# Kernel tuning notes

Measured on AMD Instinct MI355X. Metric: run time of the kernel, lower is better.

The kernel has to match this reference:

```python
import jax, jax.numpy as jnp
import numpy as np

B, H, W, DIM = 8, 64, 64, 768
NH = 12
HD = DIM // NH            # 64
WS = 14                   # window size
N = WS * WS               # 196 tokens per window
MLP = 4 * DIM             # 3072
EPS = 1e-5


def layernorm(x, w, b):
    mu = jnp.mean(x, axis=-1, keepdims=True)
    var = jnp.var(x, axis=-1, keepdims=True)
    return (x - mu) * jax.lax.rsqrt(var + EPS) * w + b


def window_partition(x, ws):
    b, h, w, c = x.shape
    pad_h = (ws - h % ws) % ws
    pad_w = (ws - w % ws) % ws
    x = jnp.pad(x, ((0, 0), (0, pad_h), (0, pad_w), (0, 0)))
    hp, wp = h + pad_h, w + pad_w
    x = x.reshape(b, hp // ws, ws, wp // ws, ws, c)
    windows = x.transpose(0, 1, 3, 2, 4, 5).reshape(-1, ws, ws, c)
    return windows, (hp, wp)


def window_unpartition(windows, ws, pad_hw, hw):
    hp, wp = pad_hw
    h, w = hw
    b = windows.shape[0] // (hp * wp // ws // ws)
    x = windows.reshape(b, hp // ws, wp // ws, ws, ws, -1)
    x = x.transpose(0, 1, 3, 2, 4, 5).reshape(b, hp, wp, -1)
    return x[:, :h, :w, :]


def setup_inputs() -> dict:
    key = jax.random.key(0)
    ks = jax.random.split(key, 8)
    f = lambda k, shape: jax.random.normal(k, shape, jnp.float32) * 0.02
    return {
        "x": jax.random.normal(ks[0], (B, H, W, DIM), jnp.float32),
        "n1_w": jnp.ones((DIM,), jnp.float32),
        "n1_b": jnp.zeros((DIM,), jnp.float32),
        "qkv_w": f(ks[1], (DIM, 3 * DIM)),
        "qkv_b": jnp.zeros((3 * DIM,), jnp.float32),
        "proj_w": f(ks[2], (DIM, DIM)),
        "proj_b": jnp.zeros((DIM,), jnp.float32),
        "rel_pos_h": f(ks[3], (2 * WS - 1, HD)),
        "rel_pos_w": f(ks[4], (2 * WS - 1, HD)),
        "n2_w": jnp.ones((DIM,), jnp.float32),
        "n2_b": jnp.zeros((DIM,), jnp.float32),
        "lin1_w": f(ks[5], (DIM, MLP)),
        "lin1_b": jnp.zeros((MLP,), jnp.float32),
        "lin2_w": f(ks[6], (MLP, DIM)),
        "lin2_b": jnp.zeros((DIM,), jnp.float32),
    }


def reference(x, n1_w, n1_b, qkv_w, qkv_b, proj_w, proj_b, rel_pos_h, rel_pos_w,
              n2_w, n2_b, lin1_w, lin1_b, lin2_w, lin2_b):
    shortcut = x
    h = layernorm(x, n1_w, n1_b)
    win, pad_hw = window_partition(h, WS)           # [Bw, WS, WS, DIM]
    bw = win.shape[0]
    qkv = win.reshape(bw, N, DIM) @ qkv_w + qkv_b   # [Bw, N, 3*DIM]
    qkv = qkv.reshape(bw, N, 3, NH, HD).transpose(2, 0, 3, 1, 4)
    qkv = qkv.reshape(3, bw * NH, N, HD)
    q, k, v = qkv[0], qkv[1], qkv[2]
    scale = HD ** -0.5
    attn = jnp.einsum('bqc,bkc->bqk', q * scale, k)  # [Bw*NH, N, N]
    # decomposed rel-pos bias; q_size == k_size == WS so no interpolation
    coords = jnp.arange(WS)[:, None] - jnp.arange(WS)[None, :] + (WS - 1)
    Rh = rel_pos_h[coords]                           # [WS, WS, HD]
    Rw = rel_pos_w[coords]
    r_q = q.reshape(-1, WS, WS, HD)
    rel_h = jnp.einsum('bhwc,hkc->bhwk', r_q, Rh)
    rel_w = jnp.einsum('bhwc,wkc->bhwk', r_q, Rw)
    attn = (attn.reshape(-1, WS, WS, WS, WS)
            + rel_h[:, :, :, :, None]
            + rel_w[:, :, :, None, :]).reshape(-1, N, N)
    attn = jax.nn.softmax(attn, axis=-1)
    out = jnp.einsum('bqk,bkc->bqc', attn, v)        # [Bw*NH, N, HD]
    out = out.reshape(bw, NH, WS, WS, HD).transpose(0, 2, 3, 1, 4)
    out = out.reshape(bw, WS, WS, DIM) @ proj_w + proj_b
    out = window_unpartition(out, WS, pad_hw, (H, W))
    x = shortcut + out
    h2 = layernorm(x, n2_w, n2_b)
    mlp = jax.nn.gelu(h2 @ lin1_w + lin1_b, approximate=False) @ lin2_w + lin2_b
    return x + mlp
```

## Files before the change

kernel.cpp:

```cpp
#include <hip/hip_runtime.h>
#include <hip/hip_bf16.h>
#include <stdint.h>

typedef __attribute__((ext_vector_type(8))) short bf16x8;
typedef __attribute__((ext_vector_type(4))) float f32x4;

__device__ __forceinline__ float bf2f(unsigned short u){
  union { unsigned int i; float f; } v; v.i = ((unsigned int)u) << 16; return v.f;
}
__device__ __forceinline__ unsigned short f2bf(float f){
  union { float f; unsigned int i; } v; v.f = f;
  return (unsigned short)((v.i + 0x7FFFu + ((v.i >> 16) & 1u)) >> 16);
}

__device__ __forceinline__ void gload16(const void* g, void* l){
  __builtin_amdgcn_global_load_lds(
      (const __attribute__((address_space(1))) void*)g,
      (__attribute__((address_space(3))) void*)l, 16, 0, 0);
}

#define VT_OFF 0L
#define Q_OFF  30720000L
#define K_OFF  60825600L

__global__ __launch_bounds__(256) void k_castT(const float* __restrict__ W,
                                               unsigned short* __restrict__ Wt,
                                               int K, int N){
  __shared__ float tl[32][33];
  int ntn = N >> 5;
  int kt = blockIdx.x / ntn, nt = blockIdx.x % ntn;
  int r = threadIdx.x >> 5, c = threadIdx.x & 31;
#pragma unroll
  for (int rr = 0; rr < 4; rr++){
    int row = (kt << 5) + r + (rr << 3);
    tl[r + (rr << 3)][c] = W[(long)row * N + (nt << 5) + c];
  }
  __syncthreads();
#pragma unroll
  for (int rr = 0; rr < 4; rr++){
    int n = (nt << 5) + r + (rr << 3);
    int k = (kt << 5) + c;
    Wt[(long)n * K + k] = f2bf(tl[c][r + (rr << 3)]);
  }
}

__global__ __launch_bounds__(256) void k_ln(const float* __restrict__ X,
                                            const float* __restrict__ w,
                                            const float* __restrict__ b,
                                            unsigned short* __restrict__ out,
                                            int mode){
  int p = blockIdx.x, t = threadIdx.x;
  unsigned short* orow = out + (long)p * 768;
  const float* xrow;
  if (mode == 1){
    int win = p / 196, tok = p - win * 196;
    int bb = win / 25, wrem = win - bb * 25;
    int wy = wrem / 5, wx = wrem - wy * 5;
    int ty = tok / 14, tx = tok - ty * 14;
    int yy = wy * 14 + ty, xx = wx * 14 + tx;
    if (yy >= 64 || xx >= 64){
      for (int j = t; j < 768; j += 256) orow[j] = 0;
      return;
    }
    xrow = X + (long)((bb * 64 + yy) * 64 + xx) * 768;
  } else {
    xrow = X + (long)p * 768;
  }
  float v0 = xrow[t], v1 = xrow[t + 256], v2 = xrow[t + 512];
  float s = v0 + v1 + v2, q = v0 * v0 + v1 * v1 + v2 * v2;
#pragma unroll
  for (int off = 32; off; off >>= 1){ s += __shfl_down(s, off); q += __shfl_down(q, off); }
  __shared__ float ps[4], pq[4], mv[2];
  int wid = t >> 6;
  if ((t & 63) == 0){ ps[wid] = s; pq[wid] = q; }
  __syncthreads();
  if (t == 0){
    float S = ps[0] + ps[1] + ps[2] + ps[3];
    float Q = pq[0] + pq[1] + pq[2] + pq[3];
    float mu = S * (1.0f / 768.0f);
    float var = Q * (1.0f / 768.0f) - mu * mu;
    mv[0] = mu; mv[1] = rsqrtf(var + 1e-5f);
  }
  __syncthreads();
  float mu = mv[0], rs = mv[1];
  orow[t]       = f2bf((v0 - mu) * rs * w[t]       + b[t]);
  orow[t + 256] = f2bf((v1 - mu) * rs * w[t + 256] + b[t + 256]);
  orow[t + 512] = f2bf((v2 - mu) * rs * w[t + 512] + b[t + 512]);
}

template<int MODE>
__global__ __launch_bounds__(256) void k_gemm(const unsigned short* __restrict__ A,
                                              const unsigned short* __restrict__ Bt,
                                              const float* bias,
                                              unsigned short* obf,
                                              float* of32,
                                              const float* addsrc,
                                              int M, int N, int K, int lda, int ldb,
                                              int tilesN){
  __shared__ __align__(16) unsigned short lA[128 * 32];
  __shared__ __align__(16) unsigned short lB[128 * 32];
  int t = threadIdx.x;

  int nwg = gridDim.x, bid = blockIdx.x;
  int qq = nwg >> 3, rr = nwg & 7;
  int xcd = bid & 7, oo = bid >> 3;
  int wg = (xcd < rr ? xcd * (qq + 1) : rr * (qq + 1) + (xcd - rr) * qq) + oo;
  int tm = wg / tilesN, tn = wg % tilesN;

  int sl = (t & 3) ^ ((t >> 3) & 3);
  const unsigned short* ga[2]; const unsigned short* gb[2];
#pragma unroll
  for (int c2 = 0; c2 < 2; c2++){
    int i = tm * 128 + c2 * 64 + (t >> 2); if (i > M - 1) i = M - 1;
    ga[c2] = A + (long)i * lda + sl * 8;
    int n = tn * 128 + c2 * 64 + (t >> 2);
    gb[c2] = Bt + (long)n * ldb + sl * 8;
  }
  unsigned short* la = lA + t * 8;
  unsigned short* lb = lB + t * 8;

  int lm = t & 15, lg = (t & 63) >> 4, wv = t >> 6;
  int wr = wv >> 1, wc = wv & 1;
  int laneoff = lm * 32 + ((lg ^ ((lm >> 1) & 3)) * 8);

  f32x4 acc[4][4];
#pragma unroll
  for (int a1 = 0; a1 < 4; a1++)
#pragma unroll
    for (int b1 = 0; b1 < 4; b1++) acc[a1][b1] = (f32x4){0.f, 0.f, 0.f, 0.f};

  for (int k0 = 0; k0 < K; k0 += 32){
    __syncthreads();
    gload16(ga[0] + k0, la);
    gload16(ga[1] + k0, la + 2048);
    gload16(gb[0] + k0, lb);
    gload16(gb[1] + k0, lb + 2048);
    __syncthreads();
    bf16x8 af[4], bfr[4];
#pragma unroll
    for (int mi = 0; mi < 4; mi++)
      af[mi] = *(const bf16x8*)(lA + (wr * 64 + mi * 16) * 32 + laneoff);
#pragma unroll
    for (int ni = 0; ni < 4; ni++)
      bfr[ni] = *(const bf16x8*)(lB + (wc * 64 + ni * 16) * 32 + laneoff);
#pragma unroll
    for (int mi = 0; mi < 4; mi++)
#pragma unroll
      for (int ni = 0; ni < 4; ni++)
        acc[mi][ni] = __builtin_amdgcn_mfma_f32_16x16x32_bf16(af[mi], bfr[ni], acc[mi][ni], 0, 0, 0);
  }

  int i0 = tm * 128 + wr * 64, j0 = tn * 128 + wc * 64;
#pragma unroll
  for (int mi = 0; mi < 4; mi++){
#pragma unroll
    for (int ni = 0; ni < 4; ni++){
      int jc = j0 + ni * 16 + lm;
      float bv = bias ? bias[jc] : 0.0f;
#pragma unroll
      for (int r = 0; r < 4; r++){
        int ir = i0 + mi * 16 + lg * 4 + r;
        float v = acc[mi][ni][r] + bv;
        if (MODE == 0){
          if (ir < M){
            int which = jc / 768, jj = jc - which * 768;
            int head = jj >> 6, cc = jj & 63;
            int win = ir / 196, tok = ir - win * 196;
            long wh = win * 12 + head;
            if (which == 0)      obf[Q_OFF + (wh * 196 + tok) * 64 + cc] = f2bf(v);
            else if (which == 1) obf[K_OFF + (wh * 196 + tok) * 64 + cc] = f2bf(v);
            else                 obf[VT_OFF + (wh * 64 + cc) * 200 + tok] = f2bf(v);
          }
        } else if (MODE == 1){
          if (ir < M){
            int win = ir / 196, tok = ir - win * 196;
            int bb = win / 25, wrem = win - bb * 25;
            int wy = wrem / 5, wx = wrem - wy * 5;
            int yy = wy * 14 + tok / 14, xx = wx * 14 + tok % 14;
            if (yy < 64 && xx < 64){
              long row = (long)((bb * 64 + yy) * 64 + xx);
              of32[row * 768 + jc] = v + addsrc[row * 768 + jc];
            }
          }
        } else if (MODE == 2){
          float g = 0.5f * v * (1.0f + erff(v * 0.70710678118654752f));
          obf[(long)ir * N + jc] = f2bf(g);
        } else {
          long idx = (long)ir * N + jc;
          of32[idx] = v + addsrc[idx];
        }
      }
    }
  }
}

#define KSW(r,c)  ((r) * 64 + ((c) ^ (((r) & 7) << 3)))
#define PSW(q,k)  ((q) * 32 + ((k) ^ (((q) & 3) << 3)))
#define DYN_ATTN  53760
__global__ __launch_bounds__(256, 2) void k_attn(const unsigned short* __restrict__ qb,
                                                 const unsigned short* __restrict__ kb,
                                                 const unsigned short* __restrict__ vtb,
                                                 const float* __restrict__ rph,
                                                 const float* __restrict__ rpw,
                                                 unsigned short* __restrict__ out){
  extern __shared__ __align__(16) char dynsm[];
  unsigned short* Ks = (unsigned short*)dynsm;
  unsigned short* Vt = (unsigned short*)(dynsm + 25088);
  __shared__ __align__(16) unsigned short Pscr[4][2][16 * 32];
  __shared__ unsigned short relhb[2744], relwb[2744];

  int t = threadIdx.x;
  int wh = blockIdx.x;
  int win = wh / 12, head = wh - win * 12;
  const unsigned short* qg  = qb  + (long)wh * 196 * 64;
  const unsigned short* kg  = kb  + (long)wh * 196 * 64;
  const unsigned short* vtg = vtb + (long)wh * 64 * 200;

  int lane = t & 63, wv = t >> 6;
  int lm = lane & 15, lg = lane >> 4;

  for (int ch = t; ch < 1568; ch += 256){
    int row = ch >> 3, c16 = ch & 7;
    gload16(kg + row * 64 + ((c16 ^ (row & 7)) << 3), (char*)Ks + ch * 16);
  }
  {
    int4 zero4 = {0, 0, 0, 0};
    for (int ch = t; ch < 1792; ch += 256){
      int row = ch / 28, c16 = ch - row * 28;
      if (c16 < 25) gload16(vtg + row * 200 + c16 * 8, (char*)Vt + ch * 16);
      else          *(int4*)((char*)Vt + ch * 16) = zero4;
    }
  }

  for (int ty = wv; ty < 14; ty += 4){
    {
      int qa = ty * 14 + lm; if (qa > 195) qa = 195;
      bf16x8 a0 = *(const bf16x8*)(&qg[qa * 64 + lg * 8]);
      bf16x8 a1 = *(const bf16x8*)(&qg[qa * 64 + 32 + lg * 8]);
      int ri = ty - lm + 13; ri = ri < 0 ? 0 : (ri > 26 ? 26 : ri);
      const float* bp = rph + ri * 64 + lg * 8;
      float4 c0 = *(const float4*)(bp),      c1 = *(const float4*)(bp + 4);
      float4 c2 = *(const float4*)(bp + 32), c3 = *(const float4*)(bp + 36);
      bf16x8 b0 = {(short)f2bf(c0.x),(short)f2bf(c0.y),(short)f2bf(c0.z),(short)f2bf(c0.w),
                   (short)f2bf(c1.x),(short)f2bf(c1.y),(short)f2bf(c1.z),(short)f2bf(c1.w)};
      bf16x8 b1 = {(short)f2bf(c2.x),(short)f2bf(c2.y),(short)f2bf(c2.z),(short)f2bf(c2.w),
                   (short)f2bf(c3.x),(short)f2bf(c3.y),(short)f2bf(c3.z),(short)f2bf(c3.w)};
      f32x4 d = (f32x4){0.f, 0.f, 0.f, 0.f};
      d = __builtin_amdgcn_mfma_f32_16x16x32_bf16(a0, b0, d, 0, 0, 0);
      d = __builtin_amdgcn_mfma_f32_16x16x32_bf16(a1, b1, d, 0, 0, 0);
#pragma unroll
      for (int r = 0; r < 4; r++){
        int txr = lg * 4 + r;
        if (txr < 14 && lm < 14) relhb[(ty * 14 + txr) * 14 + lm] = f2bf(d[r]);
      }
    }
    {
      int qa = lm * 14 + ty; if (qa > 195) qa = 195;
      bf16x8 a0 = *(const bf16x8*)(&qg[qa * 64 + lg * 8]);
      bf16x8 a1 = *(const bf16x8*)(&qg[qa * 64 + 32 + lg * 8]);
      int ri = ty - lm + 13; ri = ri < 0 ? 0 : (ri > 26 ? 26 : ri);
      const float* bp = rpw + ri * 64 + lg * 8;
      float4 c0 = *(const float4*)(bp),      c1 = *(const float4*)(bp + 4);
      float4 c2 = *(const float4*)(bp + 32), c3 = *(const float4*)(bp + 36);
      bf16x8 b0 = {(short)f2bf(c0.x),(short)f2bf(c0.y),(short)f2bf(c0.z),(short)f2bf(c0.w),
                   (short)f2bf(c1.x),(short)f2bf(c1.y),(short)f2bf(c1.z),(short)f2bf(c1.w)};
      bf16x8 b1 = {(short)f2bf(c2.x),(short)f2bf(c2.y),(short)f2bf(c2.z),(short)f2bf(c2.w),
                   (short)f2bf(c3.x),(short)f2bf(c3.y),(short)f2bf(c3.z),(short)f2bf(c3.w)};
      f32x4 d = (f32x4){0.f, 0.f, 0.f, 0.f};
      d = __builtin_amdgcn_mfma_f32_16x16x32_bf16(a0, b0, d, 0, 0, 0);
      d = __builtin_amdgcn_mfma_f32_16x16x32_bf16(a1, b1, d, 0, 0, 0);
#pragma unroll
      for (int r = 0; r < 4; r++){
        int tyr = lg * 4 + r;
        if (tyr < 14 && lm < 14) relwb[(tyr * 14 + ty) * 14 + lm] = f2bf(d[r]);
      }
    }
  }
  __syncthreads();

  int khw[13];
#pragma unroll
  for (int nt = 0; nt < 13; nt++){
    int kc = nt * 16 + lm;
    khw[nt] = (kc < 196) ? (((kc / 14) << 4) | (kc % 14)) : -1;
  }

  for (int mt = wv; mt < 13; mt += 4){
    int qr = mt * 16 + lm; if (qr > 195) qr = 195;
    bf16x8 aq0 = *(const bf16x8*)(&qg[qr * 64 + lg * 8]);
    bf16x8 aq1 = *(const bf16x8*)(&qg[qr * 64 + 32 + lg * 8]);
    f32x4 sacc[13];
#pragma unroll
    for (int nt = 0; nt < 13; nt++) sacc[nt] = (f32x4){0.f, 0.f, 0.f, 0.f};
#pragma unroll
    for (int nt = 0; nt < 13; nt++){
      int kr = nt * 16 + lm; if (kr > 195) kr = 195;
      bf16x8 bk0 = *(const bf16x8*)(&Ks[KSW(kr, lg * 8)]);
      bf16x8 bk1 = *(const bf16x8*)(&Ks[KSW(kr, 32 + lg * 8)]);
      sacc[nt] = __builtin_amdgcn_mfma_f32_16x16x32_bf16(aq0, bk0, sacc[nt], 0, 0, 0);
      sacc[nt] = __builtin_amdgcn_mfma_f32_16x16x32_bf16(aq1, bk1, sacc[nt], 0, 0, 0);
    }
    float rinv[4];
#pragma unroll
    for (int r = 0; r < 4; r++){
      int qrow = mt * 16 + lg * 4 + r;
      int qb14 = (qrow < 196) ? qrow * 14 : 0;
      float mx = -1e30f;
#pragma unroll
      for (int nt = 0; nt < 13; nt++){
        float s;
        if (khw[nt] >= 0)
          s = sacc[nt][r] * 0.125f + bf2f(relhb[qb14 + (khw[nt] >> 4)])
                                   + bf2f(relwb[qb14 + (khw[nt] & 15)]);
        else s = -1e30f;
        sacc[nt][r] = s; mx = fmaxf(mx, s);
      }
      mx = fmaxf(mx, __shfl_xor(mx, 1));
      mx = fmaxf(mx, __shfl_xor(mx, 2));
      mx = fmaxf(mx, __shfl_xor(mx, 4));
      mx = fmaxf(mx, __shfl_xor(mx, 8));
      float sum = 0.f;
#pragma unroll
      for (int nt = 0; nt < 13; nt++){
        float p = __expf(sacc[nt][r] - mx);
        sum += p;
        sacc[nt][r] = p;
      }
      sum += __shfl_xor(sum, 1); sum += __shfl_xor(sum, 2);
      sum += __shfl_xor(sum, 4); sum += __shfl_xor(sum, 8);
      rinv[r] = 1.0f / sum;
    }
    f32x4 oacc[4];
#pragma unroll
    for (int vt = 0; vt < 4; vt++) oacc[vt] = (f32x4){0.f, 0.f, 0.f, 0.f};
#pragma unroll
    for (int kk = 0; kk < 7; kk++){
      unsigned short* Ps = &Pscr[wv][kk & 1][0];
      int nt0 = 2 * kk, nt1 = 2 * kk + 1;
#pragma unroll
      for (int r = 0; r < 4; r++){
        int q = lg * 4 + r;
        Ps[PSW(q, lm)]      = f2bf(sacc[nt0][r]);
        Ps[PSW(q, lm + 16)] = (nt1 < 13) ? f2bf(sacc[nt1][r]) : (unsigned short)0;
      }
      bf16x8 ap = *(const bf16x8*)(&Ps[PSW(lm, lg * 8)]);
#pragma unroll
      for (int vt = 0; vt < 4; vt++){
        bf16x8 bv = *(const bf16x8*)(&Vt[(vt * 16 + lm) * 224 + kk * 32 + lg * 8]);
        oacc[vt] = __builtin_amdgcn_mfma_f32_16x16x32_bf16(ap, bv, oacc[vt], 0, 0, 0);
      }
    }
#pragma unroll
    for (int vt = 0; vt < 4; vt++){
#pragma unroll
      for (int r = 0; r < 4; r++){
        int orow = mt * 16 + lg * 4 + r;
        if (orow < 196)
          out[(long)(win * 196 + orow) * 768 + head * 64 + vt * 16 + lm] =
              f2bf(oacc[vt][r] * rinv[r]);
      }
    }
  }
}

static const long O_W     = 60211200;
static const long O_PROJT = 63750144;
static const long O_L1T   = 64929792;
static const long O_L2T   = 69648384;
static const long O_R2    = 74366976;
static const unsigned long WS_FULL = 275693568UL;

extern "C" void kernel_launch(void* const* d_in, const int* in_sizes, int n_in,
                              void* d_out, int out_size, void* d_ws, size_t ws_size,
                              hipStream_t stream){
  const float* x     = (const float*)d_in[0];
  const float* n1w   = (const float*)d_in[1];
  const float* n1b   = (const float*)d_in[2];
  const float* qkvw  = (const float*)d_in[3];
  const float* qkvb  = (const float*)d_in[4];
  const float* projw = (const float*)d_in[5];
  const float* projb = (const float*)d_in[6];
  const float* rph   = (const float*)d_in[7];
  const float* rpw   = (const float*)d_in[8];
  const float* n2w   = (const float*)d_in[9];
  const float* n2b   = (const float*)d_in[10];
  const float* l1w   = (const float*)d_in[11];
  const float* l1b   = (const float*)d_in[12];
  const float* l2w   = (const float*)d_in[13];
  const float* l2b   = (const float*)d_in[14];
  float* out = (float*)d_out;
  char* ws = (char*)d_ws;

  unsigned short* hpad   = (unsigned short*)(ws);
  unsigned short* attout = (unsigned short*)(ws);
  unsigned short* h2     = (unsigned short*)(ws);
  unsigned short* wqkvT  = (unsigned short*)(ws + O_W);
  unsigned short* wprojT = (unsigned short*)(ws + O_PROJT);
  unsigned short* wl1T   = (unsigned short*)(ws + O_L1T);
  unsigned short* wl2T   = (unsigned short*)(ws + O_L2T);
  unsigned short* r2     = (unsigned short*)(ws + O_R2);
  unsigned short* hidden = (unsigned short*)(ws + O_R2);

  const unsigned short* vtbuf = r2 + VT_OFF;
  const unsigned short* qbuf  = r2 + Q_OFF;
  const unsigned short* kbuf  = r2 + K_OFF;

  const bool full = (ws_size >= WS_FULL);

  k_castT<<<(768 / 32) * (2304 / 32), 256, 0, stream>>>(qkvw, wqkvT, 768, 2304);
  k_castT<<<(768 / 32) * (768 / 32),  256, 0, stream>>>(projw, wprojT, 768, 768);
  k_castT<<<(768 / 32) * (3072 / 32), 256, 0, stream>>>(l1w, wl1T, 768, 3072);
  k_castT<<<(3072 / 32) * (768 / 32), 256, 0, stream>>>(l2w, wl2T, 3072, 768);

  k_ln<<<39200, 256, 0, stream>>>(x, n1w, n1b, hpad, 1);

  k_gemm<0><<<307 * 18, 256, 0, stream>>>(hpad, wqkvT, qkvb, r2, nullptr, nullptr,
                                          39200, 2304, 768, 768, 768, 18);

  (void)hipFuncSetAttribute((const void*)k_attn,
                            hipFuncAttributeMaxDynamicSharedMemorySize, DYN_ATTN);
  k_attn<<<2400, 256, DYN_ATTN, stream>>>(qbuf, kbuf, vtbuf, rph, rpw, attout);

  k_gemm<1><<<307 * 6, 256, 0, stream>>>(attout, wprojT, projb, nullptr, out, x,
                                         39200, 768, 768, 768, 768, 6);

  k_ln<<<32768, 256, 0, stream>>>(out, n2w, n2b, h2, 0);

  if (full){
    k_gemm<2><<<256 * 24, 256, 0, stream>>>(h2, wl1T, l1b, hidden, nullptr, nullptr,
                                            32768, 3072, 768, 768, 768, 24);
    k_gemm<3><<<256 * 6, 256, 0, stream>>>(hidden, wl2T, l2b, nullptr, out, out,
                                           32768, 768, 3072, 3072, 3072, 6);
  } else {
    for (int c = 0; c < 2; c++){
      k_gemm<2><<<256 * 12, 256, 0, stream>>>(h2, wl1T + (long)c * 1536 * 768,
                                              l1b + c * 1536, hidden, nullptr, nullptr,
                                              32768, 1536, 768, 768, 768, 12);
      k_gemm<3><<<256 * 6, 256, 0, stream>>>(hidden, wl2T + c * 1536,
                                             c == 0 ? l2b : nullptr, nullptr, out, out,
                                             32768, 768, 1536, 1536, 3072, 6);
    }
  }
}
```

Measured before the change: 1.377 ms.

## Pipeline GEMM global-to-LDS loads with a 4-stage ring buffer

```diff
diff --git a/kernel.cpp b/kernel.cpp
--- a/kernel.cpp
+++ b/kernel.cpp
@@ -97,8 +97,8 @@
                                               const float* addsrc,
                                               int M, int N, int K, int lda, int ldb,
                                               int tilesN){
-  __shared__ __align__(16) unsigned short lA[128 * 32];
-  __shared__ __align__(16) unsigned short lB[128 * 32];
+  __shared__ __align__(16) unsigned short lA[4 * 128 * 32];
+  __shared__ __align__(16) unsigned short lB[4 * 128 * 32];
   int t = threadIdx.x;
 
   int nwg = gridDim.x, bid = blockIdx.x;
@@ -116,8 +116,6 @@
     int n = tn * 128 + c2 * 64 + (t >> 2);
     gb[c2] = Bt + (long)n * ldb + sl * 8;
   }
-  unsigned short* la = lA + t * 8;
-  unsigned short* lb = lB + t * 8;
 
   int lm = t & 15, lg = (t & 63) >> 4, wv = t >> 6;
   int wr = wv >> 1, wc = wv & 1;
@@ -129,20 +127,47 @@
 #pragma unroll
     for (int b1 = 0; b1 < 4; b1++) acc[a1][b1] = (f32x4){0.f, 0.f, 0.f, 0.f};
 
-  for (int k0 = 0; k0 < K; k0 += 32){
-    __syncthreads();
+  const int nt = K >> 5;
+#pragma unroll
+  for (int pt = 0; pt < 2; pt++){
+    int k0 = pt << 5;
+    unsigned short* la = lA + pt * 4096 + t * 8;
+    unsigned short* lb = lB + pt * 4096 + t * 8;
     gload16(ga[0] + k0, la);
     gload16(ga[1] + k0, la + 2048);
     gload16(gb[0] + k0, lb);
     gload16(gb[1] + k0, lb + 2048);
-    __syncthreads();
+  }
+
+  for (int tt = 0; tt < nt; tt++){
+    if (tt + 2 < nt){
+      int k0 = (tt + 2) << 5;
+      int bi = (tt + 2) & 3;
+      unsigned short* la = lA + bi * 4096 + t * 8;
+      unsigned short* lb = lB + bi * 4096 + t * 8;
+      gload16(ga[0] + k0, la);
+      gload16(ga[1] + k0, la + 2048);
+      gload16(gb[0] + k0, lb);
+      gload16(gb[1] + k0, lb + 2048);
+      asm volatile("s_waitcnt vmcnt(8)" ::: "memory");
+    } else if (tt + 1 < nt){
+      asm volatile("s_waitcnt vmcnt(4)" ::: "memory");
+    } else {
+      asm volatile("s_waitcnt vmcnt(0)" ::: "memory");
+    }
+    __builtin_amdgcn_sched_barrier(0);
+    __builtin_amdgcn_s_barrier();
+    __builtin_amdgcn_sched_barrier(0);
+
+    const unsigned short* lap = lA + (tt & 3) * 4096;
+    const unsigned short* lbp = lB + (tt & 3) * 4096;
     bf16x8 af[4], bfr[4];
 #pragma unroll
     for (int mi = 0; mi < 4; mi++)
-      af[mi] = *(const bf16x8*)(lA + (wr * 64 + mi * 16) * 32 + laneoff);
+      af[mi] = *(const bf16x8*)(lap + (wr * 64 + mi * 16) * 32 + laneoff);
 #pragma unroll
     for (int ni = 0; ni < 4; ni++)
-      bfr[ni] = *(const bf16x8*)(lB + (wc * 64 + ni * 16) * 32 + laneoff);
+      bfr[ni] = *(const bf16x8*)(lbp + (wc * 64 + ni * 16) * 32 + laneoff);
 #pragma unroll
     for (int mi = 0; mi < 4; mi++)
 #pragma unroll
```

After: 1.488 ms. +8.1%, slower.

## Double-buffer GEMM LDS tiles to overlap global loads with MFMA

Applied to the files above, without the earlier changes.

```diff
diff --git a/kernel.cpp b/kernel.cpp
--- a/kernel.cpp
+++ b/kernel.cpp
@@ -89,16 +89,16 @@
 }
 
 template<int MODE>
-__global__ __launch_bounds__(256) void k_gemm(const unsigned short* __restrict__ A,
-                                              const unsigned short* __restrict__ Bt,
-                                              const float* bias,
-                                              unsigned short* obf,
-                                              float* of32,
-                                              const float* addsrc,
-                                              int M, int N, int K, int lda, int ldb,
-                                              int tilesN){
-  __shared__ __align__(16) unsigned short lA[128 * 32];
-  __shared__ __align__(16) unsigned short lB[128 * 32];
+__global__ __launch_bounds__(256, 5) void k_gemm(const unsigned short* __restrict__ A,
+                                                 const unsigned short* __restrict__ Bt,
+                                                 const float* bias,
+                                                 unsigned short* obf,
+                                                 float* of32,
+                                                 const float* addsrc,
+                                                 int M, int N, int K, int lda, int ldb,
+                                                 int tilesN){
+  __shared__ __align__(16) unsigned short lA[2 * 128 * 32];
+  __shared__ __align__(16) unsigned short lB[2 * 128 * 32];
   int t = threadIdx.x;
 
   int nwg = gridDim.x, bid = blockIdx.x;
@@ -116,8 +116,6 @@
     int n = tn * 128 + c2 * 64 + (t >> 2);
     gb[c2] = Bt + (long)n * ldb + sl * 8;
   }
-  unsigned short* la = lA + t * 8;
-  unsigned short* lb = lB + t * 8;
 
   int lm = t & 15, lg = (t & 63) >> 4, wv = t >> 6;
   int wr = wv >> 1, wc = wv & 1;
@@ -129,25 +127,52 @@
 #pragma unroll
     for (int b1 = 0; b1 < 4; b1++) acc[a1][b1] = (f32x4){0.f, 0.f, 0.f, 0.f};
 
-  for (int k0 = 0; k0 < K; k0 += 32){
-    __syncthreads();
-    gload16(ga[0] + k0, la);
-    gload16(ga[1] + k0, la + 2048);
-    gload16(gb[0] + k0, lb);
-    gload16(gb[1] + k0, lb + 2048);
-    __syncthreads();
+  const int nt = K >> 5;
+  {
+    unsigned short* la = lA + t * 8;
+    unsigned short* lb = lB + t * 8;
+    gload16(ga[0], la);
+    gload16(ga[1], la + 2048);
+    gload16(gb[0], lb);
+    gload16(gb[1], lb + 2048);
+  }
+
+  for (int tt = 0; tt < nt; tt++){
+    int cur = tt & 1;
+    if (tt + 1 < nt){
+      int k0 = (tt + 1) << 5;
+      unsigned short* la = lA + (cur ^ 1) * 4096 + t * 8;
+      unsigned short* lb = lB + (cur ^ 1) * 4096 + t * 8;
+      gload16(ga[0] + k0, la);
+      gload16(ga[1] + k0, la + 2048);
+      gload16(gb[0] + k0, lb);
+      gload16(gb[1] + k0, lb + 2048);
+      asm volatile("s_waitcnt vmcnt(4)" ::: "memory");
+    } else {
+      asm volatile("s_waitcnt vmcnt(0)" ::: "memory");
+    }
+    __builtin_amdgcn_sched_barrier(0);
+    __builtin_amdgcn_s_barrier();
+    __builtin_amdgcn_sched_barrier(0);
+
+    const unsigned short* lap = lA + cur * 4096;
+    const unsigned short* lbp = lB + cur * 4096;
     bf16x8 af[4], bfr[4];
 #pragma unroll
     for (int mi = 0; mi < 4; mi++)
-      af[mi] = *(const bf16x8*)(lA + (wr * 64 + mi * 16) * 32 + laneoff);
+      af[mi] = *(const bf16x8*)(lap + (wr * 64 + mi * 16) * 32 + laneoff);
 #pragma unroll
     for (int ni = 0; ni < 4; ni++)
-      bfr[ni] = *(const bf16x8*)(lB + (wc * 64 + ni * 16) * 32 + laneoff);
+      bfr[ni] = *(const bf16x8*)(lbp + (wc * 64 + ni * 16) * 32 + laneoff);
+    __builtin_amdgcn_s_setprio(1);
 #pragma unroll
     for (int mi = 0; mi < 4; mi++)
 #pragma unroll
       for (int ni = 0; ni < 4; ni++)
         acc[mi][ni] = __builtin_amdgcn_mfma_f32_16x16x32_bf16(af[mi], bfr[ni], acc[mi][ni], 0, 0, 0);
+    __builtin_amdgcn_s_setprio(0);
+    __builtin_amdgcn_sched_barrier(0);
+    __builtin_amdgcn_s_barrier();
   }
 
   int i0 = tm * 128 + wr * 64, j0 = tn * 128 + wc * 64;
```

Result: slower. 3.149 ms (+128.7%).
